# Optimization experiments

Measured on AMD Instinct MI355X. Metric: run time of the kernel, lower is better.

Reference implementation:

```python
import jax, jax.numpy as jnp
import numpy as np

B, S, DIM = 8, 1, 2048
H = 16
QLR, KVLR = 1536, 512
DN, DR, DV = 128, 64, 128      # qk_nope, qk_rope, v head dims
START = 8191                    # start_pos; end_pos = START + S = 8192
EPS = 1e-6
SCALE = (DN + DR) ** -0.5


def _rms(x, w):
    # F.rms_norm: x / sqrt(mean(x^2)+eps) * w
    return x * w * jax.lax.rsqrt(jnp.mean(jnp.square(x), axis=-1, keepdims=True) + EPS)


def _rope(x, cos, sin):
    # x: [..., r]; consecutive pairs (x0,x1) treated as complex, multiplied by cos+i*sin
    xr, xi = x[..., 0::2], x[..., 1::2]
    out_r = xr * cos - xi * sin
    out_i = xr * sin + xi * cos
    return jnp.stack([out_r, out_i], axis=-1).reshape(x.shape)


def setup_inputs() -> dict:
    key = jax.random.key(0)
    ks = jax.random.split(key, 12)
    # rotary tables for the single decode position
    inv_freq = 1.0 / (10000.0 ** (np.arange(0, DR, 2, dtype=np.float32) / DR))  # [DR/2]
    pos = np.arange(START, START + S, dtype=np.float32)[:, None]                # [S,1]
    ang = pos * inv_freq[None, :]                                               # [S, DR/2]
    return {
        "x": jax.random.normal(ks[0], (B, S, DIM), jnp.float32),
        "start_pos": START,
        "freqs_cos": jnp.asarray(np.cos(ang)),
        "freqs_sin": jnp.asarray(np.sin(ang)),
        "kv_cache_prefix": jax.random.normal(ks[1], (B, START, KVLR), jnp.float32),
        "pe_cache_prefix": jax.random.normal(ks[2], (B, START, DR), jnp.float32),
        "wq_a_w": jax.random.normal(ks[3], (QLR, DIM), jnp.float32) * 0.02,
        "wq_a_b": jnp.zeros((QLR,), jnp.float32),
        "q_norm_w": jnp.ones((QLR,), jnp.float32),
        "wq_b_w": jax.random.normal(ks[4], (H * (DN + DR), QLR), jnp.float32) * 0.02,
        "wq_b_b": jnp.zeros((H * (DN + DR),), jnp.float32),
        "wkv_a_w": jax.random.normal(ks[5], (KVLR + DR, DIM), jnp.float32) * 0.02,
        "wkv_a_b": jnp.zeros((KVLR + DR,), jnp.float32),
        "kv_norm_w": jnp.ones((KVLR,), jnp.float32),
        "wkv_b_w": jax.random.normal(ks[6], (H * (DN + DV), KVLR), jnp.float32) * 0.02,
        "wo_w": jax.random.normal(ks[7], (DIM, H * DV), jnp.float32) * 0.02,
        "wo_b": jnp.zeros((DIM,), jnp.float32),
    }


def reference(x, start_pos, freqs_cos, freqs_sin, kv_cache_prefix, pe_cache_prefix,
              wq_a_w, wq_a_b, q_norm_w, wq_b_w, wq_b_b,
              wkv_a_w, wkv_a_b, kv_norm_w, wkv_b_w, wo_w, wo_b):
    b, s, _ = x.shape
    # low-rank query projection
    q = _rms(x @ wq_a_w.T + wq_a_b, q_norm_w) @ wq_b_w.T + wq_b_b
    q = q.reshape(b, s, H, DN + DR)
    q_nope, q_pe = q[..., :DN], q[..., DN:]
    cos = freqs_cos[None, :, None, :]  # [1,s,1,DR/2]
    sin = freqs_sin[None, :, None, :]
    q_pe = _rope(q_pe, cos, sin)
    # compressed KV + rope key branch
    kvpe = x @ wkv_a_w.T + wkv_a_b               # [b,s,KVLR+DR]
    kv, k_pe = kvpe[..., :KVLR], kvpe[..., KVLR:]
    k_pe = _rope(k_pe[:, :, None, :], cos, sin)[:, :, 0, :]
    # weight absorption: project q_nope into latent space through wkv_b's K-part
    wkv_b = wkv_b_w.reshape(H, DN + DV, KVLR)
    q_abs = jnp.einsum('bshd,hdc->bshc', q_nope, wkv_b[:, :DN])
    # append current step to caches
    kv_cache = jnp.concatenate([kv_cache_prefix, _rms(kv, kv_norm_w)], axis=1)  # [b,t,KVLR]
    pe_cache = jnp.concatenate([pe_cache_prefix, k_pe], axis=1)                 # [b,t,DR]
    # attention in latent space (seqlen=1 decode -> no causal mask needed)
    scores = (jnp.einsum('bshc,btc->bsht', q_abs, kv_cache)
              + jnp.einsum('bshr,btr->bsht', q_pe, pe_cache)) * SCALE
    attn = jax.nn.softmax(scores.astype(jnp.float32), axis=-1).astype(x.dtype)
    out = jnp.einsum('bsht,btc->bshc', attn, kv_cache)
    out = jnp.einsum('bshc,hdc->bshd', out, wkv_b[:, DN:])  # V-part of wkv_b
    return out.reshape(b, s, H * DV) @ wo_w.T + wo_b
```

## Files before the change

### kernel.cpp

```cpp
#include <hip/hip_runtime.h>
#include <math.h>

namespace {
constexpr int B_   = 8;
constexpr int DIM_ = 2048;
constexpr int H_   = 16;
constexpr int QLR_ = 1536;
constexpr int KVLR_= 512;
constexpr int DN_  = 128;
constexpr int DR_  = 64;
constexpr int DV_  = 128;
constexpr int TPRE_= 8191;
constexpr int CE_  = 576;
constexpr int NCH_ = 32;
constexpr int CT_  = 256;
constexpr int TS_  = 32;
constexpr int RS_  = 580;
constexpr int PSTR_= 20;
constexpr float EPS_ = 1e-6f;
constexpr float SCALE_ = 0.07216878364870322f;

constexpr size_t WS_QLAT  = 0;
constexpr size_t WS_KVPE  = WS_QLAT  + (size_t)B_*QLR_;
constexpr size_t WS_KVNEW = WS_KVPE  + (size_t)B_*CE_;
constexpr size_t WS_PENEW = WS_KVNEW + (size_t)B_*KVLR_;
constexpr size_t WS_QRS   = WS_PENEW + (size_t)B_*DR_;
constexpr size_t WS_QNOPE = WS_QRS   + (size_t)B_;
constexpr size_t WS_QT    = WS_QNOPE + (size_t)B_*H_*DN_;
constexpr size_t WS_MLOC  = WS_QT    + (size_t)B_*CE_*H_;
constexpr size_t WS_LLOC  = WS_MLOC  + (size_t)B_*H_*NCH_;
constexpr size_t WS_OUT2  = WS_LLOC  + (size_t)B_*H_*NCH_;
constexpr size_t WS_OPART = WS_OUT2  + (size_t)B_*DIM_;
}

__global__ __launch_bounds__(256) void mla_k1(const float* __restrict__ x,
                                              const float* __restrict__ wqa,
                                              const float* __restrict__ bqa,
                                              const float* __restrict__ wkva,
                                              const float* __restrict__ bkva,
                                              float* __restrict__ ws) {
  const int w = threadIdx.x >> 6, l = threadIdx.x & 63;
  const int r = blockIdx.x * 4 + w;
  const float* W; const float* bias; float* out; int rr; int ostride;
  if (r < QLR_) { W = wqa;  bias = bqa;  out = ws + WS_QLAT; rr = r;        ostride = QLR_; }
  else          { W = wkva; bias = bkva; out = ws + WS_KVPE; rr = r - QLR_; ostride = CE_;  }
  const float4* wp = (const float4*)(W + (size_t)rr * DIM_);
  const float4* x4 = (const float4*)x;
  float4 wv[8];
#pragma unroll
  for (int j = 0; j < 8; ++j) wv[j] = wp[l + 64 * j];
  float acc[B_];
#pragma unroll
  for (int b = 0; b < B_; ++b) acc[b] = 0.f;
#pragma unroll
  for (int b = 0; b < B_; ++b) {
#pragma unroll
    for (int j = 0; j < 8; ++j) {
      const float4 xv = x4[b * (DIM_ / 4) + l + 64 * j];
      acc[b] = fmaf(wv[j].x, xv.x, fmaf(wv[j].y, xv.y, fmaf(wv[j].z, xv.z, fmaf(wv[j].w, xv.w, acc[b]))));
    }
  }
#pragma unroll
  for (int b = 0; b < B_; ++b)
#pragma unroll
    for (int s = 32; s; s >>= 1) acc[b] += __shfl_xor(acc[b], s);
  if (l == 0) {
    const float b0 = bias[rr];
#pragma unroll
    for (int b = 0; b < B_; ++b) out[b * ostride + rr] = acc[b] + b0;
  }
}

__global__ __launch_bounds__(256) void mla_k2(const float* __restrict__ kvnw,
                                              const float* __restrict__ fcos,
                                              const float* __restrict__ fsin,
                                              float* __restrict__ ws) {
  const int tid = threadIdx.x;
  const int b = tid >> 5, i = tid & 31;
  const float* kvpe = ws + WS_KVPE + b * CE_;
  float ss = 0.f;
#pragma unroll
  for (int j = 0; j < KVLR_ / 32; ++j) { const float v = kvpe[i + 32 * j]; ss = fmaf(v, v, ss); }
#pragma unroll
  for (int s = 16; s; s >>= 1) ss += __shfl_xor(ss, s, 32);
  const float scale = 1.0f / sqrtf(ss / (float)KVLR_ + EPS_);
  float* kvn = ws + WS_KVNEW + b * KVLR_;
#pragma unroll
  for (int j = 0; j < KVLR_ / 32; ++j) {
    const int c = i + 32 * j;
    kvn[c] = kvpe[c] * kvnw[c] * scale;
  }
  {
    const float xr = kvpe[KVLR_ + 2 * i], xi = kvpe[KVLR_ + 2 * i + 1];
    const float c = fcos[i], s = fsin[i];
    float* pen = ws + WS_PENEW + b * DR_;
    pen[2 * i]     = xr * c - xi * s;
    pen[2 * i + 1] = xr * s + xi * c;
  }
  {
    const float* p = ws + WS_QLAT + b * QLR_;
    float sq = 0.f;
#pragma unroll
    for (int j = 0; j < QLR_ / 32; ++j) { const float v = p[i + 32 * j]; sq = fmaf(v, v, sq); }
#pragma unroll
    for (int s = 16; s; s >>= 1) sq += __shfl_xor(sq, s, 32);
    if (i == 0) ws[WS_QRS + b] = 1.0f / sqrtf(sq / (float)QLR_ + EPS_);
  }
}

__global__ __launch_bounds__(256) void mla_k3(const float* __restrict__ qnw,
                                              const float* __restrict__ wqb,
                                              const float* __restrict__ bqb,
                                              const float* __restrict__ fcos,
                                              const float* __restrict__ fsin,
                                              float* __restrict__ ws) {
  const int w = threadIdx.x >> 6, l = threadIdx.x & 63;
  const int r0 = blockIdx.x * 8 + w * 2;
  const float4* w0p = (const float4*)(wqb + (size_t)r0 * QLR_);
  const float4* w1p = (const float4*)(wqb + (size_t)(r0 + 1) * QLR_);
  const float4* g4  = (const float4*)qnw;
  const float4* x4  = (const float4*)(ws + WS_QLAT);
  float4 wg0[6], wg1[6];
#pragma unroll
  for (int j = 0; j < 6; ++j) {
    const int c4 = l + 64 * j;
    const float4 a = w0p[c4], bb = w1p[c4], g = g4[c4];
    wg0[j].x = a.x * g.x; wg0[j].y = a.y * g.y; wg0[j].z = a.z * g.z; wg0[j].w = a.w * g.w;
    wg1[j].x = bb.x * g.x; wg1[j].y = bb.y * g.y; wg1[j].z = bb.z * g.z; wg1[j].w = bb.w * g.w;
  }
  float acc0[B_], acc1[B_];
#pragma unroll
  for (int b = 0; b < B_; ++b) { acc0[b] = 0.f; acc1[b] = 0.f; }
#pragma unroll
  for (int b = 0; b < B_; ++b) {
#pragma unroll
    for (int j = 0; j < 6; ++j) {
      const float4 xv = x4[b * (QLR_ / 4) + l + 64 * j];
      acc0[b] = fmaf(wg0[j].x, xv.x, fmaf(wg0[j].y, xv.y, fmaf(wg0[j].z, xv.z, fmaf(wg0[j].w, xv.w, acc0[b]))));
      acc1[b] = fmaf(wg1[j].x, xv.x, fmaf(wg1[j].y, xv.y, fmaf(wg1[j].z, xv.z, fmaf(wg1[j].w, xv.w, acc1[b]))));
    }
  }
#pragma unroll
  for (int b = 0; b < B_; ++b)
#pragma unroll
    for (int s = 32; s; s >>= 1) {
      acc0[b] += __shfl_xor(acc0[b], s);
      acc1[b] += __shfl_xor(acc1[b], s);
    }
  if (l == 0) {
    const int h = r0 / (DN_ + DR_);
    const int j0 = r0 - h * (DN_ + DR_);
    const float b0 = bqb[r0], b1 = bqb[r0 + 1];
    if (j0 < DN_) {
      float* qn = ws + WS_QNOPE;
#pragma unroll
      for (int b = 0; b < B_; ++b) {
        const float sb = ws[WS_QRS + b];
        qn[(b * H_ + h) * DN_ + j0]     = acc0[b] * sb + b0;
        qn[(b * H_ + h) * DN_ + j0 + 1] = acc1[b] * sb + b1;
      }
    } else {
      const int i = (j0 - DN_) >> 1;
      const float c = fcos[i], s = fsin[i];
      float* qT = ws + WS_QT;
#pragma unroll
      for (int b = 0; b < B_; ++b) {
        const float sb = ws[WS_QRS + b];
        const float xr = acc0[b] * sb + b0, xi = acc1[b] * sb + b1;
        qT[((size_t)b * CE_ + KVLR_ + 2 * i) * H_ + h]     = xr * c - xi * s;
        qT[((size_t)b * CE_ + KVLR_ + 2 * i + 1) * H_ + h] = xr * s + xi * c;
      }
    }
  }
}

__global__ __launch_bounds__(256) void mla_k4(const float* __restrict__ wkvb,
                                              float* __restrict__ ws) {
  __shared__ float red[7 * 32 * B_];
  const int h = blockIdx.y;
  const int strip = blockIdx.x;
  const int tid = threadIdx.x;
  const int c = tid & 31, dg = tid >> 5;
  const int cg = strip * 32 + c;
  const float* qn = ws + WS_QNOPE;
  float acc[B_];
#pragma unroll
  for (int b = 0; b < B_; ++b) acc[b] = 0.f;
  const float* wp = wkvb + (size_t)h * 256 * KVLR_ + cg;
#pragma unroll
  for (int dd = 0; dd < 16; ++dd) {
    const int d = dg * 16 + dd;
    const float wv = wp[(size_t)d * KVLR_];
#pragma unroll
    for (int b = 0; b < B_; ++b) acc[b] = fmaf(qn[(b * H_ + h) * DN_ + d], wv, acc[b]);
  }
  if (dg > 0) {
#pragma unroll
    for (int b = 0; b < B_; ++b) red[(((dg - 1) * 32) + c) * B_ + b] = acc[b];
  }
  __syncthreads();
  if (dg == 0) {
    float* qT = ws + WS_QT;
#pragma unroll
    for (int b = 0; b < B_; ++b) {
      float v = acc[b];
#pragma unroll
      for (int g = 0; g < 7; ++g) v += red[(g * 32 + c) * B_ + b];
      qT[((size_t)b * CE_ + cg) * H_ + h] = v;
    }
  }
}

__global__ __launch_bounds__(512, 2) void mla_k5(const float* __restrict__ kvpre,
                                                 const float* __restrict__ pepre,
                                                 float* __restrict__ ws) {
  __shared__ float kv_lds[TS_ * RS_];
  __shared__ float q_lds[H_ * RS_];
  __shared__ float p_lds[TS_ * PSTR_];
  __shared__ float m_st[H_], l_st[H_], f_st[H_];

  const int b = blockIdx.y;
  const int chunk = blockIdx.x;
  const int t0 = chunk * CT_;
  const int tid = threadIdx.x;

  {
    const float4* qsrc = (const float4*)(ws + WS_QT + (size_t)b * CE_ * H_);
#pragma unroll
    for (int it = 0; it < 5; ++it) {
      const int idx = tid + 512 * it;
      if (idx < (CE_ * H_) / 4) {
        const float4 v = qsrc[idx];
        const int c = idx >> 2, h4 = (idx & 3) * 4;
        q_lds[(h4 + 0) * RS_ + c] = v.x;
        q_lds[(h4 + 1) * RS_ + c] = v.y;
        q_lds[(h4 + 2) * RS_ + c] = v.z;
        q_lds[(h4 + 3) * RS_ + c] = v.w;
      }
    }
    if (tid < H_) { m_st[tid] = -3.4e38f; l_st[tid] = 0.f; }
  }

  int fr[9], fw[9];
#pragma unroll
  for (int i = 0; i < 9; ++i) {
    const int f = tid + 512 * i;
    fr[i] = f / 144; fw[i] = f % 144;
  }
  const float* kvnew = ws + WS_KVNEW + b * KVLR_;
  const float* penew = ws + WS_PENEW + b * DR_;

  float4 stg[9];
  auto loadR = [&](int ts) {
#pragma unroll
    for (int i = 0; i < 9; ++i) {
      const int t = t0 + ts * TS_ + fr[i];
      const int wi = fw[i];
      const float* src;
      if (t < TPRE_) {
        src = (wi < 128) ? (kvpre + ((size_t)b * TPRE_ + t) * KVLR_ + wi * 4)
                         : (pepre + ((size_t)b * TPRE_ + t) * DR_ + (wi - 128) * 4);
      } else {
        src = (wi < 128) ? (kvnew + wi * 4) : (penew + (wi - 128) * 4);
      }
      stg[i] = *(const float4*)src;
    }
  };
  loadR(0);

  float o[H_];
#pragma unroll
  for (int h = 0; h < H_; ++h) o[h] = 0.f;

  const int t_sc = tid >> 4, h_sc = tid & 15;
  const int h2 = tid >> 5, tg = tid & 31;

  for (int ts = 0; ts < CT_ / TS_; ++ts) {
    __syncthreads();
#pragma unroll
    for (int i = 0; i < 9; ++i)
      *(float4*)(kv_lds + fr[i] * RS_ + fw[i] * 4) = stg[i];
    if (ts + 1 < CT_ / TS_) loadR(ts + 1);
    __syncthreads();

    {
      const float4* kr = (const float4*)(kv_lds + t_sc * RS_);
      const float4* qr = (const float4*)(q_lds + h_sc * RS_);
      float ax = 0.f, ay = 0.f, az = 0.f, aw = 0.f;
#pragma unroll
      for (int c4 = 0; c4 < 144; ++c4) {
        const float4 k = kr[c4], q = qr[c4];
        ax = fmaf(k.x, q.x, ax); ay = fmaf(k.y, q.y, ay);
        az = fmaf(k.z, q.z, az); aw = fmaf(k.w, q.w, aw);
      }
      p_lds[t_sc * PSTR_ + h_sc] = (ax + ay + az + aw) * SCALE_;
    }
    __syncthreads();

    {
      const float s = p_lds[tg * PSTR_ + h2];
      float msub = s;
#pragma unroll
      for (int d = 16; d; d >>= 1) msub = fmaxf(msub, __shfl_xor(msub, d, 32));
      const float mold = m_st[h2];
      const float mnew = fmaxf(mold, msub);
      const float e = __expf(s - mnew);
      float lsum = e;
#pragma unroll
      for (int d = 16; d; d >>= 1) lsum += __shfl_xor(lsum, d, 32);
      p_lds[tg * PSTR_ + h2] = e;
      if (tg == 0) {
        const float fac = __expf(mold - mnew);
        f_st[h2] = fac;
        l_st[h2] = l_st[h2] * fac + lsum;
        m_st[h2] = mnew;
      }
    }
    __syncthreads();

    {
      const int c = tid;
      const float4 f0 = *(const float4*)&f_st[0];
      const float4 f1 = *(const float4*)&f_st[4];
      const float4 f2 = *(const float4*)&f_st[8];
      const float4 f3 = *(const float4*)&f_st[12];
      o[0] *= f0.x; o[1] *= f0.y; o[2] *= f0.z; o[3] *= f0.w;
      o[4] *= f1.x; o[5] *= f1.y; o[6] *= f1.z; o[7] *= f1.w;
      o[8] *= f2.x; o[9] *= f2.y; o[10] *= f2.z; o[11] *= f2.w;
      o[12] *= f3.x; o[13] *= f3.y; o[14] *= f3.z; o[15] *= f3.w;
#pragma unroll 8
      for (int t = 0; t < TS_; ++t) {
        const float kvv = kv_lds[t * RS_ + c];
        const float4 p0 = *(const float4*)(p_lds + t * PSTR_);
        const float4 p1 = *(const float4*)(p_lds + t * PSTR_ + 4);
        const float4 p2 = *(const float4*)(p_lds + t * PSTR_ + 8);
        const float4 p3 = *(const float4*)(p_lds + t * PSTR_ + 12);
        o[0]  = fmaf(p0.x, kvv, o[0]);  o[1]  = fmaf(p0.y, kvv, o[1]);
        o[2]  = fmaf(p0.z, kvv, o[2]);  o[3]  = fmaf(p0.w, kvv, o[3]);
        o[4]  = fmaf(p1.x, kvv, o[4]);  o[5]  = fmaf(p1.y, kvv, o[5]);
        o[6]  = fmaf(p1.z, kvv, o[6]);  o[7]  = fmaf(p1.w, kvv, o[7]);
        o[8]  = fmaf(p2.x, kvv, o[8]);  o[9]  = fmaf(p2.y, kvv, o[9]);
        o[10] = fmaf(p2.z, kvv, o[10]); o[11] = fmaf(p2.w, kvv, o[11]);
        o[12] = fmaf(p3.x, kvv, o[12]); o[13] = fmaf(p3.y, kvv, o[13]);
        o[14] = fmaf(p3.z, kvv, o[14]); o[15] = fmaf(p3.w, kvv, o[15]);
      }
    }
  }

  {
    const int c = tid;
    float* Op = ws + WS_OPART + ((size_t)(b * H_) * NCH_ + chunk) * KVLR_;
#pragma unroll
    for (int h = 0; h < H_; ++h)
      Op[(size_t)h * NCH_ * KVLR_ + c] = o[h];
    if (tid < H_) {
      ws[WS_MLOC + (b * H_ + tid) * NCH_ + chunk] = m_st[tid];
      ws[WS_LLOC + (b * H_ + tid) * NCH_ + chunk] = l_st[tid];
    }
  }
}

__global__ __launch_bounds__(256) void mla_k6(const float* __restrict__ wkvb,
                                              float* __restrict__ ws) {
  const int h = blockIdx.x, b = blockIdx.y;
  __shared__ float wgt[NCH_];
  __shared__ float ao[KVLR_];
  __shared__ float Linv;
  const int tid = threadIdx.x;
  if (tid < NCH_) {
    const float m = ws[WS_MLOC + (b * H_ + h) * NCH_ + tid];
    float M = m;
#pragma unroll
    for (int s = 16; s; s >>= 1) M = fmaxf(M, __shfl_xor(M, s, 32));
    const float wv = __expf(m - M);
    wgt[tid] = wv;
    float lv = ws[WS_LLOC + (b * H_ + h) * NCH_ + tid] * wv;
#pragma unroll
    for (int s = 16; s; s >>= 1) lv += __shfl_xor(lv, s, 32);
    if (tid == 0) Linv = 1.0f / lv;
  }
  __syncthreads();
  const float* Ob = ws + WS_OPART + (size_t)(b * H_ + h) * NCH_ * KVLR_;
  float s0 = 0.f, s1 = 0.f;
#pragma unroll 4
  for (int i = 0; i < NCH_; ++i) {
    const float wv = wgt[i];
    s0 = fmaf(wv, Ob[(size_t)i * KVLR_ + tid], s0);
    s1 = fmaf(wv, Ob[(size_t)i * KVLR_ + tid + 256], s1);
  }
  const float li = Linv;
  ao[tid] = s0 * li;
  ao[tid + 256] = s1 * li;
  __syncthreads();
  const int v = tid >> 1, half = tid & 1;
  const float* w2 = wkvb + ((size_t)h * 256 + DN_ + v) * KVLR_ + half * 256;
  const float* a = ao + half * 256;
  float s = 0.f;
#pragma unroll
  for (int c = 0; c < 256; c += 4) {
    const float4 wv = *(const float4*)(w2 + c);
    s = fmaf(wv.x, a[c], s);
    s = fmaf(wv.y, a[c + 1], s);
    s = fmaf(wv.z, a[c + 2], s);
    s = fmaf(wv.w, a[c + 3], s);
  }
  s += __shfl_xor(s, 1);
  if (half == 0) ws[WS_OUT2 + b * DIM_ + h * DV_ + v] = s;
}

__global__ __launch_bounds__(256) void mla_k7(const float* __restrict__ wo,
                                              const float* __restrict__ wob,
                                              const float* __restrict__ ws,
                                              float* __restrict__ out) {
  const int w = threadIdx.x >> 6, l = threadIdx.x & 63;
  const int r = blockIdx.x * 4 + w;
  const float4* wp = (const float4*)(wo + (size_t)r * DIM_);
  const float4* x4 = (const float4*)(ws + WS_OUT2);
  float4 wv[8];
#pragma unroll
  for (int j = 0; j < 8; ++j) wv[j] = wp[l + 64 * j];
  float acc[B_];
#pragma unroll
  for (int b = 0; b < B_; ++b) acc[b] = 0.f;
#pragma unroll
  for (int b = 0; b < B_; ++b) {
#pragma unroll
    for (int j = 0; j < 8; ++j) {
      const float4 xv = x4[b * (DIM_ / 4) + l + 64 * j];
      acc[b] = fmaf(wv[j].x, xv.x, fmaf(wv[j].y, xv.y, fmaf(wv[j].z, xv.z, fmaf(wv[j].w, xv.w, acc[b]))));
    }
  }
#pragma unroll
  for (int b = 0; b < B_; ++b)
#pragma unroll
    for (int s = 32; s; s >>= 1) acc[b] += __shfl_xor(acc[b], s);
  if (l == 0) {
    const float b0 = wob[r];
#pragma unroll
    for (int b = 0; b < B_; ++b) out[b * DIM_ + r] = acc[b] + b0;
  }
}

extern "C" void kernel_launch(void* const* d_in, const int* in_sizes, int n_in,
                              void* d_out, int out_size, void* d_ws, size_t ws_size,
                              hipStream_t stream) {
  (void)in_sizes; (void)n_in; (void)out_size; (void)ws_size;
  const float* x     = (const float*)d_in[0];
  const float* fcos  = (const float*)d_in[2];
  const float* fsin  = (const float*)d_in[3];
  const float* kvpre = (const float*)d_in[4];
  const float* pepre = (const float*)d_in[5];
  const float* wqa   = (const float*)d_in[6];
  const float* bqa   = (const float*)d_in[7];
  const float* qnw   = (const float*)d_in[8];
  const float* wqb   = (const float*)d_in[9];
  const float* bqb   = (const float*)d_in[10];
  const float* wkva  = (const float*)d_in[11];
  const float* bkva  = (const float*)d_in[12];
  const float* kvnw  = (const float*)d_in[13];
  const float* wkvb  = (const float*)d_in[14];
  const float* wo    = (const float*)d_in[15];
  const float* wob   = (const float*)d_in[16];
  float* ws  = (float*)d_ws;
  float* out = (float*)d_out;

  mla_k1<<<dim3((QLR_ + CE_) / 4), dim3(256), 0, stream>>>(x, wqa, bqa, wkva, bkva, ws);
  mla_k2<<<dim3(1), dim3(256), 0, stream>>>(kvnw, fcos, fsin, ws);
  mla_k3<<<dim3(H_ * (DN_ + DR_) / 8), dim3(256), 0, stream>>>(qnw, wqb, bqb, fcos, fsin, ws);
  mla_k4<<<dim3(16, H_), dim3(256), 0, stream>>>(wkvb, ws);
  mla_k5<<<dim3(NCH_, B_), dim3(512), 0, stream>>>(kvpre, pepre, ws);
  mla_k6<<<dim3(H_, B_), dim3(256), 0, stream>>>(wkvb, ws);
  mla_k7<<<dim3(DIM_ / 4), dim3(256), 0, stream>>>(wo, wob, ws, out);
}
```

Baseline: 426.6 us.

## Double-buffer KV tiles via async global-to-LDS loads and register-tile attention

The decode attention kernel now stages each 16-token KV/PE tile directly into one of two LDS buffers with global_load_lds, so the next tile streams in while the current one is processed. Register staging and the padded row layout are removed. The QK score step splits the latent dimension across 8 lanes with shuffle reductions and computes a 2-token by 4-head tile per thread from a head-interleaved q layout. The PV step uses a 4x4 register tile of columns by heads with float4 LDS reads. The goal is to hide global latency and cut LDS traffic per FMA. The risks are that only half the threads do the score and softmax work, and that the smaller tile means more barriers per chunk.

```diff
diff --git a/kernel.cpp b/kernel.cpp
--- a/kernel.cpp
+++ b/kernel.cpp
@@ -14,8 +14,7 @@
 constexpr int CE_  = 576;
 constexpr int NCH_ = 32;
 constexpr int CT_  = 256;
-constexpr int TS_  = 32;
-constexpr int RS_  = 580;
+constexpr int TS_  = 16;
 constexpr int PSTR_= 20;
 constexpr float EPS_ = 1e-6f;
 constexpr float SCALE_ = 0.07216878364870322f;
@@ -31,6 +30,12 @@
 constexpr size_t WS_LLOC  = WS_MLOC  + (size_t)B_*H_*NCH_;
 constexpr size_t WS_OUT2  = WS_LLOC  + (size_t)B_*H_*NCH_;
 constexpr size_t WS_OPART = WS_OUT2  + (size_t)B_*DIM_;
+}
+
+__device__ __forceinline__ void gload16(const float* src, float* ldsDst) {
+  __builtin_amdgcn_global_load_lds((const __attribute__((address_space(1))) void*)src,
+                                   (__attribute__((address_space(3))) void*)ldsDst,
+                                   16, 0, 0);
 }
 
 __global__ __launch_bounds__(256) void mla_k1(const float* __restrict__ x,
@@ -214,8 +219,8 @@
 __global__ __launch_bounds__(512, 2) void mla_k5(const float* __restrict__ kvpre,
                                                  const float* __restrict__ pepre,
                                                  float* __restrict__ ws) {
-  __shared__ float kv_lds[TS_ * RS_];
-  __shared__ float q_lds[H_ * RS_];
+  __shared__ float kv_lds[2][TS_ * CE_];
+  __shared__ float q_lds[9248];
   __shared__ float p_lds[TS_ * PSTR_];
   __shared__ float m_st[H_], l_st[H_], f_st[H_];
 
@@ -223,91 +228,116 @@
   const int chunk = blockIdx.x;
   const int t0 = chunk * CT_;
   const int tid = threadIdx.x;
+  const int w = tid >> 6, l = tid & 63;
+  const float* kvnew = ws + WS_KVNEW + b * KVLR_;
+  const float* penew = ws + WS_PENEW + b * DR_;
+
+  auto stageKV = [&](float* buf, int s) {
+    const int ts0 = t0 + s * TS_;
+    for (int i = w; i < (TS_ * CE_) / 256; i += 8) {
+      const int f = i * 64 + l;
+      const int tl = f / 144;
+      const int c4 = f - tl * 144;
+      const int tg = ts0 + tl;
+      const float* src;
+      if (tg < TPRE_) {
+        src = (c4 < 128) ? (kvpre + ((size_t)b * TPRE_ + tg) * KVLR_ + 4 * c4)
+                         : (pepre + ((size_t)b * TPRE_ + tg) * DR_ + 4 * (c4 - 128));
+      } else {
+        src = (c4 < 128) ? (kvnew + 4 * c4) : (penew + 4 * (c4 - 128));
+      }
+      gload16(src, buf + (size_t)i * 256);
+    }
+  };
+
+  stageKV(kv_lds[0], 0);
 
   {
     const float4* qsrc = (const float4*)(ws + WS_QT + (size_t)b * CE_ * H_);
 #pragma unroll
-    for (int it = 0; it < 5; ++it) {
-      const int idx = tid + 512 * it;
+    for (int k = 0; k < 5; ++k) {
+      const int idx = tid + 512 * k;
       if (idx < (CE_ * H_) / 4) {
         const float4 v = qsrc[idx];
-        const int c = idx >> 2, h4 = (idx & 3) * 4;
-        q_lds[(h4 + 0) * RS_ + c] = v.x;
-        q_lds[(h4 + 1) * RS_ + c] = v.y;
-        q_lds[(h4 + 2) * RS_ + c] = v.z;
-        q_lds[(h4 + 3) * RS_ + c] = v.w;
+        const int c = idx >> 2, hq = idx & 3;
+        *(float4*)(q_lds + c * 16 + hq * 4 + 4 * (c / 72)) = v;
       }
     }
     if (tid < H_) { m_st[tid] = -3.4e38f; l_st[tid] = 0.f; }
   }
 
-  int fr[9], fw[9];
-#pragma unroll
-  for (int i = 0; i < 9; ++i) {
-    const int f = tid + 512 * i;
-    fr[i] = f / 144; fw[i] = f % 144;
-  }
-  const float* kvnew = ws + WS_KVNEW + b * KVLR_;
-  const float* penew = ws + WS_PENEW + b * DR_;
-
-  float4 stg[9];
-  auto loadR = [&](int ts) {
-#pragma unroll
-    for (int i = 0; i < 9; ++i) {
-      const int t = t0 + ts * TS_ + fr[i];
-      const int wi = fw[i];
-      const float* src;
-      if (t < TPRE_) {
-        src = (wi < 128) ? (kvpre + ((size_t)b * TPRE_ + t) * KVLR_ + wi * 4)
-                         : (pepre + ((size_t)b * TPRE_ + t) * DR_ + (wi - 128) * 4);
-      } else {
-        src = (wi < 128) ? (kvnew + wi * 4) : (penew + (wi - 128) * 4);
-      }
-      stg[i] = *(const float4*)src;
-    }
-  };
-  loadR(0);
-
-  float o[H_];
-#pragma unroll
-  for (int h = 0; h < H_; ++h) o[h] = 0.f;
-
-  const int t_sc = tid >> 4, h_sc = tid & 15;
-  const int h2 = tid >> 5, tg = tid & 31;
-
-  for (int ts = 0; ts < CT_ / TS_; ++ts) {
+  const int c8 = l >> 3;
+  const int rlo = l & 7;
+  const int t2 = ((w & 3) << 1) + (rlo >> 2);
+  const int h4 = rlo & 3;
+  const int c4p = tid >> 2, h4p = tid & 3;
+
+  float o[4][4];
+#pragma unroll
+  for (int cc = 0; cc < 4; ++cc)
+#pragma unroll
+    for (int hh = 0; hh < 4; ++hh) o[cc][hh] = 0.f;
+
+  for (int s = 0; s < CT_ / TS_; ++s) {
     __syncthreads();
-#pragma unroll
-    for (int i = 0; i < 9; ++i)
-      *(float4*)(kv_lds + fr[i] * RS_ + fw[i] * 4) = stg[i];
-    if (ts + 1 < CT_ / TS_) loadR(ts + 1);
+    if (s + 1 < CT_ / TS_) stageKV(kv_lds[(s + 1) & 1], s + 1);
+    const float* bufc = kv_lds[s & 1];
+
+    if (tid < 256) {
+      const float* r0 = bufc + (2 * t2) * CE_ + c8 * 72;
+      const float* r1 = r0 + CE_;
+      const float* qb = q_lds + (c8 * 72) * 16 + 4 * c8 + 4 * h4;
+      float acc0[4] = {0.f, 0.f, 0.f, 0.f};
+      float acc1[4] = {0.f, 0.f, 0.f, 0.f};
+#pragma unroll
+      for (int j = 0; j < 18; ++j) {
+        const float4 k0 = *(const float4*)(r0 + 4 * j);
+        const float4 k1 = *(const float4*)(r1 + 4 * j);
+        const float4 q0 = *(const float4*)(qb + (4 * j + 0) * 16);
+        const float4 q1 = *(const float4*)(qb + (4 * j + 1) * 16);
+        const float4 q2 = *(const float4*)(qb + (4 * j + 2) * 16);
+        const float4 q3 = *(const float4*)(qb + (4 * j + 3) * 16);
+        acc0[0] = fmaf(k0.x, q0.x, fmaf(k0.y, q1.x, fmaf(k0.z, q2.x, fmaf(k0.w, q3.x, acc0[0]))));
+        acc0[1] = fmaf(k0.x, q0.y, fmaf(k0.y, q1.y, fmaf(k0.z, q2.y, fmaf(k0.w, q3.y, acc0[1]))));
+        acc0[2] = fmaf(k0.x, q0.z, fmaf(k0.y, q1.z, fmaf(k0.z, q2.z, fmaf(k0.w, q3.z, acc0[2]))));
+        acc0[3] = fmaf(k0.x, q0.w, fmaf(k0.y, q1.w, fmaf(k0.z, q2.w, fmaf(k0.w, q3.w, acc0[3]))));
+        acc1[0] = fmaf(k1.x, q0.x, fmaf(k1.y, q1.x, fmaf(k1.z, q2.x, fmaf(k1.w, q3.x, acc1[0]))));
+        acc1[1] = fmaf(k1.x, q0.y, fmaf(k1.y, q1.y, fmaf(k1.z, q2.y, fmaf(k1.w, q3.y, acc1[1]))));
+        acc1[2] = fmaf(k1.x, q0.z, fmaf(k1.y, q1.z, fmaf(k1.z, q2.z, fmaf(k1.w, q3.z, acc1[2]))));
+        acc1[3] = fmaf(k1.x, q0.w, fmaf(k1.y, q1.w, fmaf(k1.z, q2.w, fmaf(k1.w, q3.w, acc1[3]))));
+      }
+#pragma unroll
+      for (int d = 8; d <= 32; d <<= 1) {
+#pragma unroll
+        for (int hh = 0; hh < 4; ++hh) {
+          acc0[hh] += __shfl_xor(acc0[hh], d);
+          acc1[hh] += __shfl_xor(acc1[hh], d);
+        }
+      }
+      if (c8 == 0) {
+        float4 v0, v1;
+        v0.x = acc0[0] * SCALE_; v0.y = acc0[1] * SCALE_;
+        v0.z = acc0[2] * SCALE_; v0.w = acc0[3] * SCALE_;
+        v1.x = acc1[0] * SCALE_; v1.y = acc1[1] * SCALE_;
+        v1.z = acc1[2] * SCALE_; v1.w = acc1[3] * SCALE_;
+        *(float4*)(p_lds + (2 * t2) * PSTR_ + 4 * h4)     = v0;
+        *(float4*)(p_lds + (2 * t2 + 1) * PSTR_ + 4 * h4) = v1;
+      }
+    }
     __syncthreads();
 
-    {
-      const float4* kr = (const float4*)(kv_lds + t_sc * RS_);
-      const float4* qr = (const float4*)(q_lds + h_sc * RS_);
-      float ax = 0.f, ay = 0.f, az = 0.f, aw = 0.f;
-#pragma unroll
-      for (int c4 = 0; c4 < 144; ++c4) {
-        const float4 k = kr[c4], q = qr[c4];
-        ax = fmaf(k.x, q.x, ax); ay = fmaf(k.y, q.y, ay);
-        az = fmaf(k.z, q.z, az); aw = fmaf(k.w, q.w, aw);
-      }
-      p_lds[t_sc * PSTR_ + h_sc] = (ax + ay + az + aw) * SCALE_;
-    }
-    __syncthreads();
-
-    {
-      const float s = p_lds[tg * PSTR_ + h2];
-      float msub = s;
-#pragma unroll
-      for (int d = 16; d; d >>= 1) msub = fmaxf(msub, __shfl_xor(msub, d, 32));
+    if (tid < 256) {
+      const int h2 = tid >> 4, tg = tid & 15;
+      const float sv = p_lds[tg * PSTR_ + h2];
+      float msub = sv;
+#pragma unroll
+      for (int d = 1; d < 16; d <<= 1) msub = fmaxf(msub, __shfl_xor(msub, d, 16));
       const float mold = m_st[h2];
       const float mnew = fmaxf(mold, msub);
-      const float e = __expf(s - mnew);
+      const float e = __expf(sv - mnew);
       float lsum = e;
 #pragma unroll
-      for (int d = 16; d; d >>= 1) lsum += __shfl_xor(lsum, d, 32);
+      for (int d = 1; d < 16; d <<= 1) lsum += __shfl_xor(lsum, d, 16);
       p_lds[tg * PSTR_ + h2] = e;
       if (tg == 0) {
         const float fac = __expf(mold - mnew);
@@ -319,40 +349,36 @@
     __syncthreads();
 
     {
-      const int c = tid;
-      const float4 f0 = *(const float4*)&f_st[0];
-      const float4 f1 = *(const float4*)&f_st[4];
-      const float4 f2 = *(const float4*)&f_st[8];
-      const float4 f3 = *(const float4*)&f_st[12];
-      o[0] *= f0.x; o[1] *= f0.y; o[2] *= f0.z; o[3] *= f0.w;
-      o[4] *= f1.x; o[5] *= f1.y; o[6] *= f1.z; o[7] *= f1.w;
-      o[8] *= f2.x; o[9] *= f2.y; o[10] *= f2.z; o[11] *= f2.w;
-      o[12] *= f3.x; o[13] *= f3.y; o[14] *= f3.z; o[15] *= f3.w;
-#pragma unroll 8
+      const float4 fv = *(const float4*)(f_st + 4 * h4p);
+#pragma unroll
+      for (int cc = 0; cc < 4; ++cc) {
+        o[cc][0] *= fv.x; o[cc][1] *= fv.y; o[cc][2] *= fv.z; o[cc][3] *= fv.w;
+      }
+#pragma unroll
       for (int t = 0; t < TS_; ++t) {
-        const float kvv = kv_lds[t * RS_ + c];
-        const float4 p0 = *(const float4*)(p_lds + t * PSTR_);
-        const float4 p1 = *(const float4*)(p_lds + t * PSTR_ + 4);
-        const float4 p2 = *(const float4*)(p_lds + t * PSTR_ + 8);
-        const float4 p3 = *(const float4*)(p_lds + t * PSTR_ + 12);
-        o[0]  = fmaf(p0.x, kvv, o[0]);  o[1]  = fmaf(p0.y, kvv, o[1]);
-        o[2]  = fmaf(p0.z, kvv, o[2]);  o[3]  = fmaf(p0.w, kvv, o[3]);
-        o[4]  = fmaf(p1.x, kvv, o[4]);  o[5]  = fmaf(p1.y, kvv, o[5]);
-        o[6]  = fmaf(p1.z, kvv, o[6]);  o[7]  = fmaf(p1.w, kvv, o[7]);
-        o[8]  = fmaf(p2.x, kvv, o[8]);  o[9]  = fmaf(p2.y, kvv, o[9]);
-        o[10] = fmaf(p2.z, kvv, o[10]); o[11] = fmaf(p2.w, kvv, o[11]);
-        o[12] = fmaf(p3.x, kvv, o[12]); o[13] = fmaf(p3.y, kvv, o[13]);
-        o[14] = fmaf(p3.z, kvv, o[14]); o[15] = fmaf(p3.w, kvv, o[15]);
+        const float4 kq = *(const float4*)(bufc + t * CE_ + 4 * c4p);
+        const float4 pq = *(const float4*)(p_lds + t * PSTR_ + 4 * h4p);
+        o[0][0] = fmaf(pq.x, kq.x, o[0][0]); o[0][1] = fmaf(pq.y, kq.x, o[0][1]);
+        o[0][2] = fmaf(pq.z, kq.x, o[0][2]); o[0][3] = fmaf(pq.w, kq.x, o[0][3]);
+        o[1][0] = fmaf(pq.x, kq.y, o[1][0]); o[1][1] = fmaf(pq.y, kq.y, o[1][1]);
+        o[1][2] = fmaf(pq.z, kq.y, o[1][2]); o[1][3] = fmaf(pq.w, kq.y, o[1][3]);
+        o[2][0] = fmaf(pq.x, kq.z, o[2][0]); o[2][1] = fmaf(pq.y, kq.z, o[2][1]);
+        o[2][2] = fmaf(pq.z, kq.z, o[2][2]); o[2][3] = fmaf(pq.w, kq.z, o[2][3]);
+        o[3][0] = fmaf(pq.x, kq.w, o[3][0]); o[3][1] = fmaf(pq.y, kq.w, o[3][1]);
+        o[3][2] = fmaf(pq.z, kq.w, o[3][2]); o[3][3] = fmaf(pq.w, kq.w, o[3][3]);
       }
     }
   }
 
   {
-    const int c = tid;
-    float* Op = ws + WS_OPART + ((size_t)(b * H_) * NCH_ + chunk) * KVLR_;
-#pragma unroll
-    for (int h = 0; h < H_; ++h)
-      Op[(size_t)h * NCH_ * KVLR_ + c] = o[h];
+    float* Op = ws + WS_OPART;
+#pragma unroll
+    for (int hh = 0; hh < 4; ++hh) {
+      const int h = 4 * h4p + hh;
+      float4 v;
+      v.x = o[0][hh]; v.y = o[1][hh]; v.z = o[2][hh]; v.w = o[3][hh];
+      *(float4*)(Op + ((size_t)(b * H_ + h) * NCH_ + chunk) * KVLR_ + 4 * c4p) = v;
+    }
     if (tid < H_) {
       ws[WS_MLOC + (b * H_ + tid) * NCH_ + chunk] = m_st[tid];
       ws[WS_LLOC + (b * H_ + tid) * NCH_ + chunk] = l_st[tid];
```

Measured after the change: 366.6 us. 1.16x faster.
